# Kernel optimization log

Hardware: AMD Instinct MI355X
Metric: run time of the kernel (lower is better)

## Reference

```python
import jax, jax.numpy as jnp
import numpy as np


def _pairwise_adj(x):
    # exp(-||xi - xj||^2), shape [B, N, N]
    inner = -2.0 * jnp.einsum('bnd,bmd->bnm', x, x)
    sq = jnp.sum(x * x, axis=-1, keepdims=True)
    return jnp.exp(-(sq + inner + jnp.swapaxes(sq, 1, 2)))


def _knn_adj(adj, k):
    # keep top-k weights per row, zero elsewhere
    vals, idx = jax.lax.top_k(adj, k)
    b = jnp.arange(adj.shape[0])[:, None, None]
    n = jnp.arange(adj.shape[1])[None, :, None]
    return jnp.zeros_like(adj).at[b, n, idx].set(vals)


def _laplacian(adj):
    # normalized Laplacian L = I - D^-1/2 A D^-1/2
    d = jnp.sum(adj, axis=-1)
    dinv = jnp.where(d > 0, 1.0 / jnp.sqrt(d), 0.0)
    norm_adj = dinv[:, :, None] * adj * dinv[:, None, :]
    return jnp.eye(adj.shape[1], dtype=adj.dtype) - norm_adj


def _cheb_conv(x, L, W, b):
    # Chebyshev polynomial graph conv: sum_k T_k(L) x W_k + b
    K = W.shape[0]
    x0 = x
    out = jnp.einsum('bnf,fo->bno', x0, W[0])
    if K > 1:
        x1 = jnp.matmul(L, x0)
        out = out + jnp.einsum('bnf,fo->bno', x1, W[1])
        for kk in range(2, K):
            x2 = 2.0 * jnp.matmul(L, x1) - x0
            out = out + jnp.einsum('bnf,fo->bno', x2, W[kk])
            x0, x1 = x1, x2
    return out + b


def setup_inputs() -> dict:
    key = jax.random.key(0)
    ks = jax.random.split(key, 4)
    B, N, Fin, Fout, K, C = 16, 2048, 6, 128, 6, 40
    x = jax.random.normal(ks[0], (B, N, Fin), dtype=jnp.float32)
    sccs = jax.random.randint(ks[1], (B, 64, 16), 0, N)  # unused in one_layer branch
    W1 = jax.random.normal(ks[2], (K, Fin, Fout), dtype=jnp.float32) * 0.05
    b1 = jnp.zeros((Fout,), dtype=jnp.float32)
    fc_w = jax.random.normal(ks[3], (Fout, C), dtype=jnp.float32) * 0.05
    fc_b = jnp.zeros((C,), dtype=jnp.float32)
    return {"x": x, "k": 40, "batch_size": B, "num_points": N,
            "sccs": sccs, "W1": W1, "b1": b1, "fc_w": fc_w, "fc_b": fc_b}


def reference(x, k, batch_size, num_points, sccs, W1, b1, fc_w, fc_b):
    # graph built under no_grad in the original -> stop_gradient here
    L = jax.lax.stop_gradient(_laplacian(_knn_adj(_pairwise_adj(x), k)))
    out = jax.nn.relu(_cheb_conv(x, L, W1, b1))           # [B, N, 128]
    # reg_prior: ||out^T L out||_F ** 2
    M = jnp.einsum('bnf,bnm,bmg->bfg', out, L, out)       # [B, 128, 128]
    reg = jnp.sum(M * M)
    pooled = jnp.max(out, axis=1)                         # [B, 128]
    logits = pooled @ fc_w + fc_b                         # [B, class_num]
    return logits, reg
```

## Files before the change

### kernel.cpp

```cpp
#include <hip/hip_runtime.h>
#include <math.h>

#define BB   16
#define NN   2048
#define FIN  6
#define FOUT 128
#define KCH  6
#define KNN  40
#define NCLS 40

__global__ __launch_bounds__(512) void knn_kernel(const float* __restrict__ x,
                                                  int* __restrict__ topi,
                                                  float* __restrict__ topv,
                                                  float* __restrict__ dinv)
{
    __shared__ __align__(16) float xs[FIN][NN];
    __shared__ unsigned int   hist[8][64];
    __shared__ unsigned int   ck[8][64];
    __shared__ unsigned short ci[8][64];
    __shared__ unsigned int   ccnt[8];

    int bb   = blockIdx.x >> 5;
    int i0   = (blockIdx.x & 31) * 64;
    int t    = threadIdx.x;
    int lane = t & 63;
    int wv   = t >> 6;

    const float* xb = x + (size_t)bb * NN * FIN;
    for (int idx = t; idx < NN * FIN; idx += 512) {
        int j = idx / FIN, f = idx - j * FIN;
        xs[f][j] = xb[idx];
    }
    __syncthreads();

    for (int rr = 0; rr < 8; ++rr) {
        int i   = i0 + wv * 8 + rr;
        int row = bb * NN + i;

        float xi0 = xs[0][i], xi1 = xs[1][i], xi2 = xs[2][i],
              xi3 = xs[3][i], xi4 = xs[4][i], xi5 = xs[5][i];

        float d[32];
#pragma unroll
        for (int uu = 0; uu < 8; ++uu) {
            int j4 = uu * 64 + lane;
            float4 p0 = ((const float4*)xs[0])[j4];
            float4 p1 = ((const float4*)xs[1])[j4];
            float4 p2 = ((const float4*)xs[2])[j4];
            float4 p3 = ((const float4*)xs[3])[j4];
            float4 p4 = ((const float4*)xs[4])[j4];
            float4 p5 = ((const float4*)xs[5])[j4];
#define DNE(E, C)                                                                \
            { float q0 = p0.C - xi0, q1 = p1.C - xi1, q2 = p2.C - xi2,           \
                    q3 = p3.C - xi3, q4 = p4.C - xi4, q5 = p5.C - xi5;           \
              d[uu * 4 + E] = fmaf(q5,q5, fmaf(q4,q4, fmaf(q3,q3,                \
                              fmaf(q2,q2, fmaf(q1,q1, q0*q0)))));  }
            DNE(0, x) DNE(1, y) DNE(2, z) DNE(3, w)
#undef DNE
        }

        float lo = 0.0f, invw = 16.0f;
        int base = 0, pivot = 127;

        for (int pass = 0; pass < 6; ++pass) {
            hist[wv][lane] = 0u;
#pragma unroll
            for (int u = 0; u < 32; ++u) {
                float dv = d[u];
                if (dv >= lo) {
                    int bin = (int)((dv - lo) * invw);
                    if (bin < 128)
                        atomicAdd(&hist[wv][bin >> 1], 1u << ((bin & 1) << 4));
                }
            }
            unsigned int h = hist[wv][lane];
            int b0 = (int)(h & 0xFFFFu), b1 = (int)(h >> 16);
            int s = b0 + b1;
            int incl = s;
#pragma unroll
            for (int off = 1; off < 64; off <<= 1) {
                int up = __shfl_up(incl, off, 64);
                if (lane >= off) incl += up;
            }
            int total = __shfl(incl, 63, 64);

            if (base + total < KNN) {
                base += total;
                lo   += 128.0f / invw;
                invw *= 0.5f;
                continue;
            }

            unsigned long long ball = __ballot(base + incl >= KNN);
            int pl = __ffsll(ball) - 1;
            int p_ = 0, cb_ = 0, cs_ = 0;
            if (lane == pl) {
                int cbefore = base + incl - s;
                if (cbefore + b0 >= KNN) { p_ = pl * 2;     cb_ = cbefore;      cs_ = cbefore + b0; }
                else                     { p_ = pl * 2 + 1; cb_ = cbefore + b0; cs_ = cbefore + b0 + b1; }
            }
            pivot    = __shfl(p_, pl, 64);
            int cumb = __shfl(cb_, pl, 64);
            int csel = __shfl(cs_, pl, 64);

            if (csel <= 64) break;

            lo   = lo + (float)pivot / invw;
            invw *= 128.0f;
            base = cumb;
        }

        if (lane == 0) ccnt[wv] = 0u;
#pragma unroll
        for (int u = 0; u < 32; ++u) {
            int ib = (int)((d[u] - lo) * invw);
            if (ib <= pivot) {
                unsigned int slot = atomicAdd(&ccnt[wv], 1u);
                if (slot < 64u) {
                    ck[wv][slot] = __float_as_uint(d[u]);
                    ci[wv][slot] = (unsigned short)((u >> 2) * 256 + (lane << 2) + (u & 3));
                }
            }
        }
        unsigned int c = ccnt[wv];
        if (c > 64u) c = 64u;

        unsigned int kk = (lane < (int)c) ? ck[wv][lane] : 0xFFFFFFFFu;
        int          id = (lane < (int)c) ? (int)ci[wv][lane] : -1;

        int rank = 0;
        int cI = (int)c;
        for (int m = 0; m < cI; ++m) {
            unsigned int km = __shfl(kk, m, 64);
            rank += (km < kk || (km == kk && m < lane)) ? 1 : 0;
        }

        float ev = 0.0f;
        if (rank < KNN) {
            ev = expf(-__uint_as_float(kk));
            topv[(size_t)row * KNN + rank] = ev;
            topi[(size_t)row * KNN + rank] = id;
        }
        float ssum = ev;
#pragma unroll
        for (int off = 32; off; off >>= 1) ssum += __shfl_xor(ssum, off, 64);
        if (lane == 0) dinv[row] = 1.0f / sqrtf(ssum);
    }
}

__global__ __launch_bounds__(192) void cheb_apply(const float* __restrict__ xin,
                                                  const float* __restrict__ xsub,
                                                  float* __restrict__ xout,
                                                  const int* __restrict__ topi,
                                                  const float* __restrict__ wnrm,
                                                  const float* __restrict__ topv,
                                                  const float* __restrict__ dinv,
                                                  float* __restrict__ wnrm_out,
                                                  float scale)
{
    __shared__ int   si[32 * KNN];
    __shared__ float sw[32 * KNN];
    int r0 = blockIdx.x * 32;
    int t  = threadIdx.x;
    if (topv) {
        int b = r0 >> 11;
        const float* dv = dinv + ((size_t)b << 11);
        for (int l = t; l < 32 * KNN; l += 192) {
            size_t idx = (size_t)r0 * KNN + l;
            int j = topi[idx];
            float w = topv[idx] * dinv[r0 + l / KNN] * dv[j];
            si[l] = j; sw[l] = w;
            wnrm_out[idx] = w;
        }
    } else {
        for (int l = t; l < 32 * KNN; l += 192) {
            si[l] = topi[(size_t)r0 * KNN + l];
            sw[l] = wnrm[(size_t)r0 * KNN + l];
        }
    }
    __syncthreads();

    int rl = t / FIN, f = t - rl * FIN;
    int r  = r0 + rl;
    int b  = r >> 11;
    const float* xbase = xin + (size_t)b * NN * FIN + f;
    const int*   sip = si + rl * KNN;
    const float* swp = sw + rl * KNN;
    float a = xin[(size_t)r * FIN + f];
#pragma unroll 8
    for (int s = 0; s < KNN; ++s)
        a = fmaf(-swp[s], xbase[(size_t)sip[s] * FIN], a);
    a *= scale;
    if (xsub) a -= xsub[(size_t)r * FIN + f];
    xout[(size_t)r * FIN + f] = a;
}

__global__ __launch_bounds__(512) void chebout_kernel(const float* __restrict__ x,
                                                      const float* __restrict__ xks,
                                                      const float* __restrict__ W1,
                                                      const float* __restrict__ b1,
                                                      float* __restrict__ outb,
                                                      float* __restrict__ pmax)
{
    __shared__ float W1s[KCH * FIN * FOUT];
    __shared__ float b1s[FOUT];
    __shared__ float xk[16][KCH * FIN];
    __shared__ float mx[4][FOUT];
    int r0 = blockIdx.x * 16;
    int t  = threadIdx.x;
    for (int l = t; l < KCH * FIN * FOUT; l += 512) W1s[l] = W1[l];
    if (t < FOUT) b1s[t] = b1[t];
    for (int l = t; l < 16 * KCH * FIN; l += 512) {
        int rl = l / (KCH * FIN), kf = l % (KCH * FIN);
        int k = kf / FIN, f = kf % FIN;
        int r = r0 + rl;
        xk[rl][kf] = (k == 0) ? x[(size_t)r * FIN + f]
                              : xks[(size_t)(k - 1) * BB * NN * FIN + (size_t)r * FIN + f];
    }
    __syncthreads();
    int fo = t & 127;
    float om = 0.0f;
#pragma unroll
    for (int it = 0; it < 4; ++it) {
        int rl = (t >> 7) + it * 4;
        float acc = b1s[fo];
#pragma unroll
        for (int kf = 0; kf < KCH * FIN; ++kf)
            acc = fmaf(xk[rl][kf], W1s[kf * FOUT + fo], acc);
        float o = fmaxf(acc, 0.0f);
        outb[(size_t)(r0 + rl) * FOUT + fo] = o;
        om = fmaxf(om, o);
    }
    mx[t >> 7][fo] = om;
    __syncthreads();
    if (t < FOUT) {
        float m = fmaxf(fmaxf(mx[0][t], mx[1][t]), fmaxf(mx[2][t], mx[3][t]));
        int b = r0 >> 11;
        atomicMax((unsigned int*)&pmax[(size_t)b * FOUT + t], __float_as_uint(m));
    }
}

__global__ __launch_bounds__(1024) void loutmsq_kernel(const float* __restrict__ outb,
                                                       const int* __restrict__ topi,
                                                       const float* __restrict__ wnrm,
                                                       float* __restrict__ mchunk)
{
    int id  = blockIdx.x;
    int xcd = id & 7, k = id >> 3;
    int bb  = xcd + 8 * (k >> 4);
    int nch = k & 15;
    int t   = threadIdx.x;

    __shared__ __align__(16) float aT[64][FOUT];
    __shared__ __align__(16) float bT[64][FOUT];

    const float* ob = outb + (size_t)bb * NN * FOUT;
    float acc[4][4] = {{0.f}};
    int tx = t & 31, ty = t >> 5;
    int grl = t >> 4;
    int gfq = (t & 15) * 2;

    for (int st = 0; st < 2; ++st) {
        int n0 = nch * 128 + st * 64;
        {
            const float4* src = (const float4*)(ob + (size_t)n0 * FOUT);
            float4* dst = (float4*)aT;
            dst[t]        = src[t];
            dst[t + 1024] = src[t + 1024];
        }
        __syncthreads();
        {
            int r = n0 + grl;
            const int*   ti = topi + ((size_t)bb * NN + r) * KNN;
            const float* tw = wnrm + ((size_t)bb * NN + r) * KNN;
            float4 a0 = ((const float4*)aT[grl])[gfq];
            float4 a1 = ((const float4*)aT[grl])[gfq + 1];
#pragma unroll 8
            for (int s = 0; s < KNN; ++s) {
                int j = ti[s]; float w = tw[s];
                const float4* jr = (const float4*)(ob + (size_t)j * FOUT);
                float4 v0 = jr[gfq], v1 = jr[gfq + 1];
                a0.x = fmaf(-w, v0.x, a0.x); a0.y = fmaf(-w, v0.y, a0.y);
                a0.z = fmaf(-w, v0.z, a0.z); a0.w = fmaf(-w, v0.w, a0.w);
                a1.x = fmaf(-w, v1.x, a1.x); a1.y = fmaf(-w, v1.y, a1.y);
                a1.z = fmaf(-w, v1.z, a1.z); a1.w = fmaf(-w, v1.w, a1.w);
            }
            ((float4*)bT[grl])[gfq]     = a0;
            ((float4*)bT[grl])[gfq + 1] = a1;
        }
        __syncthreads();
#pragma unroll 8
        for (int qq = 0; qq < 64; ++qq) {
            float4 av = ((const float4*)aT[qq])[tx];
            float4 bv = ((const float4*)bT[qq])[ty];
            float af[4] = {av.x, av.y, av.z, av.w};
            float bg[4] = {bv.x, bv.y, bv.z, bv.w};
#pragma unroll
            for (int ii = 0; ii < 4; ++ii)
#pragma unroll
                for (int jj = 0; jj < 4; ++jj)
                    acc[ii][jj] = fmaf(af[ii], bg[jj], acc[ii][jj]);
        }
        __syncthreads();
    }
    size_t basem = ((size_t)bb * 16 + nch) << 14;
#pragma unroll
    for (int ii = 0; ii < 4; ++ii) {
        float4 v = make_float4(acc[ii][0], acc[ii][1], acc[ii][2], acc[ii][3]);
        *(float4*)&mchunk[basem + (size_t)(tx * 4 + ii) * FOUT + ty * 4] = v;
    }
}

__global__ __launch_bounds__(256) void mred_kernel(const float* __restrict__ mchunk,
                                                   float* __restrict__ mpart)
{
    int t = threadIdx.x;
    size_t E = ((size_t)blockIdx.x * 256 + t) * 4;
    int bb = (int)(E >> 14);
    int fg = (int)(E & 16383);
    float4 a = make_float4(0.f, 0.f, 0.f, 0.f);
    for (int c = 0; c < 16; ++c) {
        float4 v = *(const float4*)&mchunk[((size_t)(bb * 16 + c) << 14) + fg];
        a.x += v.x; a.y += v.y; a.z += v.z; a.w += v.w;
    }
    float s = a.x * a.x + a.y * a.y + a.z * a.z + a.w * a.w;
#pragma unroll
    for (int off = 32; off; off >>= 1) s += __shfl_down(s, off, 64);
    __shared__ float ws[4];
    if ((t & 63) == 0) ws[t >> 6] = s;
    __syncthreads();
    if (t == 0) mpart[blockIdx.x] = ws[0] + ws[1] + ws[2] + ws[3];
}

__global__ __launch_bounds__(128) void logits_kernel(const float* __restrict__ pmax,
                                                     const float* __restrict__ fcw,
                                                     const float* __restrict__ fcb,
                                                     const float* __restrict__ mpart,
                                                     float* __restrict__ dout)
{
    int b = blockIdx.x, t = threadIdx.x;
    if (b == BB) {
        float s = mpart[t] + mpart[t + 128];
#pragma unroll
        for (int off = 32; off; off >>= 1) s += __shfl_down(s, off, 64);
        __shared__ float ws[2];
        if ((t & 63) == 0) ws[t >> 6] = s;
        __syncthreads();
        if (t == 0) dout[BB * NCLS] = ws[0] + ws[1];
        return;
    }
    __shared__ float pooled[FOUT];
    pooled[t] = pmax[(size_t)b * FOUT + t];
    __syncthreads();
    if (t < NCLS) {
        float acc = fcb[t];
        for (int f = 0; f < FOUT; ++f) acc = fmaf(pooled[f], fcw[f * NCLS + t], acc);
        dout[b * NCLS + t] = acc;
    }
}

extern "C" void kernel_launch(void* const* d_in, const int* in_sizes, int n_in,
                              void* d_out, int out_size, void* d_ws, size_t ws_size,
                              hipStream_t stream)
{
    const float* x   = (const float*)d_in[0];
    const float* W1  = (const float*)d_in[5];
    const float* b1  = (const float*)d_in[6];
    const float* fcw = (const float*)d_in[7];
    const float* fcb = (const float*)d_in[8];

    char* p = (char*)d_ws;
    auto alloc = [&](size_t bytes) { void* q = (void*)p; p += (bytes + 255) & ~(size_t)255; return q; };
    int*   topi   = (int*)  alloc((size_t)BB * NN * KNN * 4);
    float* topv   = (float*)alloc((size_t)BB * NN * KNN * 4);
    float* dinv   = (float*)alloc((size_t)BB * NN * 4);
    float* wnrm   = (float*)alloc((size_t)BB * NN * KNN * 4);
    float* xks    = (float*)alloc((size_t)5 * BB * NN * FIN * 4);
    float* outb   = (float*)alloc((size_t)BB * NN * FOUT * 4);
    float* mchunk = (float*)alloc((size_t)BB * 16 * FOUT * FOUT * 4);
    float* mpart  = (float*)alloc(256 * 4);
    float* pmax   = (float*)alloc((size_t)BB * FOUT * 4);

    const size_t ST = (size_t)BB * NN * FIN;

    hipMemsetAsync(pmax, 0, (size_t)BB * FOUT * 4, stream);

    knn_kernel<<<512, 512, 0, stream>>>(x, topi, topv, dinv);

    cheb_apply<<<1024, 192, 0, stream>>>(x,            nullptr,      xks + 0 * ST, topi, nullptr, topv, dinv, wnrm, 1.0f);
    cheb_apply<<<1024, 192, 0, stream>>>(xks + 0 * ST, x,            xks + 1 * ST, topi, wnrm, nullptr, nullptr, nullptr, 2.0f);
    cheb_apply<<<1024, 192, 0, stream>>>(xks + 1 * ST, xks + 0 * ST, xks + 2 * ST, topi, wnrm, nullptr, nullptr, nullptr, 2.0f);
    cheb_apply<<<1024, 192, 0, stream>>>(xks + 2 * ST, xks + 1 * ST, xks + 3 * ST, topi, wnrm, nullptr, nullptr, nullptr, 2.0f);
    cheb_apply<<<1024, 192, 0, stream>>>(xks + 3 * ST, xks + 2 * ST, xks + 4 * ST, topi, wnrm, nullptr, nullptr, nullptr, 2.0f);

    chebout_kernel<<<BB * NN / 16, 512, 0, stream>>>(x, xks, W1, b1, outb, pmax);
    loutmsq_kernel<<<256, 1024, 0, stream>>>(outb, topi, wnrm, mchunk);
    mred_kernel<<<256, 256, 0, stream>>>(mchunk, mpart);
    logits_kernel<<<BB + 1, 128, 0, stream>>>(pmax, fcw, fcb, mpart, (float*)d_out);
}
```

Baseline: 226.7 us.

## Fuse five Chebyshev recurrence launches into one cooperative kernel with grid syncs

Replaces the five separate cheb_apply launches with a single cooperative kernel that loads the neighbor indices and normalized weights into shared memory once, then runs all five recurrence steps with grid.sync between them. The pmax memset is folded into the same kernel. This is meant to remove launch overhead and repeated neighbor and weight loads, at the cost of grid-wide barriers and the requirement that all 1024 blocks be co-resident.

After: 713.0 us. +214.5%, slower.

```diff
diff --git a/kernel.cpp b/kernel.cpp
--- a/kernel.cpp
+++ b/kernel.cpp
@@ -1,5 +1,8 @@
 #include <hip/hip_runtime.h>
+#include <hip/hip_cooperative_groups.h>
 #include <math.h>
+
+namespace cg = cooperative_groups;
 
 #define BB   16
 #define NN   2048
@@ -148,21 +151,23 @@
     }
 }
 
-__global__ __launch_bounds__(192) void cheb_apply(const float* __restrict__ xin,
-                                                  const float* __restrict__ xsub,
-                                                  float* __restrict__ xout,
-                                                  const int* __restrict__ topi,
-                                                  const float* __restrict__ wnrm,
-                                                  const float* __restrict__ topv,
-                                                  const float* __restrict__ dinv,
-                                                  float* __restrict__ wnrm_out,
-                                                  float scale)
-{
+__global__ __launch_bounds__(192) void cheb_all_kernel(const float* __restrict__ x,
+                                                       float* __restrict__ xks,
+                                                       const int* __restrict__ topi,
+                                                       const float* __restrict__ topv,
+                                                       const float* __restrict__ dinv,
+                                                       float* __restrict__ wnrm,
+                                                       float* __restrict__ pmax)
+{
+    cg::grid_group grid = cg::this_grid();
     __shared__ int   si[32 * KNN];
     __shared__ float sw[32 * KNN];
     int r0 = blockIdx.x * 32;
     int t  = threadIdx.x;
-    if (topv) {
+
+    if (blockIdx.x < BB && t < FOUT) pmax[blockIdx.x * FOUT + t] = 0.0f;
+
+    {
         int b = r0 >> 11;
         const float* dv = dinv + ((size_t)b << 11);
         for (int l = t; l < 32 * KNN; l += 192) {
@@ -170,12 +175,7 @@
             int j = topi[idx];
             float w = topv[idx] * dinv[r0 + l / KNN] * dv[j];
             si[l] = j; sw[l] = w;
-            wnrm_out[idx] = w;
-        }
-    } else {
-        for (int l = t; l < 32 * KNN; l += 192) {
-            si[l] = topi[(size_t)r0 * KNN + l];
-            sw[l] = wnrm[(size_t)r0 * KNN + l];
+            wnrm[idx] = w;
         }
     }
     __syncthreads();
@@ -183,16 +183,27 @@
     int rl = t / FIN, f = t - rl * FIN;
     int r  = r0 + rl;
     int b  = r >> 11;
-    const float* xbase = xin + (size_t)b * NN * FIN + f;
+    const size_t ST = (size_t)BB * NN * FIN;
     const int*   sip = si + rl * KNN;
     const float* swp = sw + rl * KNN;
-    float a = xin[(size_t)r * FIN + f];
+
+    for (int k = 1; k <= 5; ++k) {
+        const float* xin  = (k == 1) ? x : xks + (size_t)(k - 2) * ST;
+        const float* xsub = (k == 1) ? nullptr : ((k == 2) ? x : xks + (size_t)(k - 3) * ST);
+        float*       xout = xks + (size_t)(k - 1) * ST;
+        float scale = (k == 1) ? 1.0f : 2.0f;
+
+        const float* xbase = xin + (size_t)b * NN * FIN + f;
+        float a = xin[(size_t)r * FIN + f];
 #pragma unroll 8
-    for (int s = 0; s < KNN; ++s)
-        a = fmaf(-swp[s], xbase[(size_t)sip[s] * FIN], a);
-    a *= scale;
-    if (xsub) a -= xsub[(size_t)r * FIN + f];
-    xout[(size_t)r * FIN + f] = a;
+        for (int s = 0; s < KNN; ++s)
+            a = fmaf(-swp[s], xbase[(size_t)sip[s] * FIN], a);
+        a *= scale;
+        if (xsub) a -= xsub[(size_t)r * FIN + f];
+        xout[(size_t)r * FIN + f] = a;
+
+        if (k < 5) grid.sync();
+    }
 }
 
 __global__ __launch_bounds__(512) void chebout_kernel(const float* __restrict__ x,
@@ -381,17 +392,15 @@
     float* mpart  = (float*)alloc(256 * 4);
     float* pmax   = (float*)alloc((size_t)BB * FOUT * 4);
 
-    const size_t ST = (size_t)BB * NN * FIN;
-
-    hipMemsetAsync(pmax, 0, (size_t)BB * FOUT * 4, stream);
-
     knn_kernel<<<512, 512, 0, stream>>>(x, topi, topv, dinv);
 
-    cheb_apply<<<1024, 192, 0, stream>>>(x,            nullptr,      xks + 0 * ST, topi, nullptr, topv, dinv, wnrm, 1.0f);
-    cheb_apply<<<1024, 192, 0, stream>>>(xks + 0 * ST, x,            xks + 1 * ST, topi, wnrm, nullptr, nullptr, nullptr, 2.0f);
-    cheb_apply<<<1024, 192, 0, stream>>>(xks + 1 * ST, xks + 0 * ST, xks + 2 * ST, topi, wnrm, nullptr, nullptr, nullptr, 2.0f);
-    cheb_apply<<<1024, 192, 0, stream>>>(xks + 2 * ST, xks + 1 * ST, xks + 3 * ST, topi, wnrm, nullptr, nullptr, nullptr, 2.0f);
-    cheb_apply<<<1024, 192, 0, stream>>>(xks + 3 * ST, xks + 2 * ST, xks + 4 * ST, topi, wnrm, nullptr, nullptr, nullptr, 2.0f);
+    {
+        void* cx = (void*)x;
+        void* args[] = { (void*)&cx, (void*)&xks, (void*)&topi, (void*)&topv,
+                         (void*)&dinv, (void*)&wnrm, (void*)&pmax };
+        hipLaunchCooperativeKernel((const void*)cheb_all_kernel,
+                                   dim3(1024), dim3(192), args, 0, stream);
+    }
 
     chebout_kernel<<<BB * NN / 16, 512, 0, stream>>>(x, xks, W1, b1, outb, pmax);
     loutmsq_kernel<<<256, 1024, 0, stream>>>(outb, topi, wnrm, mchunk);
```
